# Kernel optimization log

Measured on AMD Instinct MI355X. Metric: run time of the kernel, lower is better.

The kernel has to match this reference:

```python
import jax, jax.numpy as jnp
import numpy as np

DIM = 32
ED = DIM * DIM          # 1024
HID = ED * 4            # 4096
EPS = 1e-5


def _ln(x, g, b):
    # LayerNorm over last two dims (d, d)
    m = x.mean(axis=(-2, -1), keepdims=True)
    v = jnp.var(x, axis=(-2, -1), keepdims=True)
    return (x - m) * jax.lax.rsqrt(v + EPS) * g + b


def setup_inputs() -> dict:
    key = jax.random.key(0)
    ks = jax.random.split(key, 10)
    b, s, d = 2, 1024, DIM
    inp = {
        "x": jax.random.normal(ks[0], (b, s, d, d), dtype=jnp.float32),
        # StateSpaceLayer params
        "log_A": jax.random.normal(ks[1], (d,), dtype=jnp.float32) * 0.02,
        "w_dt": jax.random.normal(ks[2], (d,), dtype=jnp.float32) / np.sqrt(d),
        "b_dt": jnp.zeros((), dtype=jnp.float32),
        "g_ssm": jnp.ones((d, d), dtype=jnp.float32),
        "b_ssm": jnp.zeros((d, d), dtype=jnp.float32),
        # FFN params
        "g_ffn": jnp.ones((d, d), dtype=jnp.float32),
        "b_ffn": jnp.zeros((d, d), dtype=jnp.float32),
        "W1": jax.random.normal(ks[3], (ED, HID), dtype=jnp.float32) / np.sqrt(ED),
        "bb1": jnp.zeros((HID,), dtype=jnp.float32),
        "W2": jax.random.normal(ks[4], (HID, ED), dtype=jnp.float32) / np.sqrt(HID),
        "bb2": jnp.zeros((ED,), dtype=jnp.float32),
    }
    return inp


def reference(x, log_A, w_dt, b_dt, g_ssm, b_ssm, g_ffn, b_ffn, W1, bb1, W2, bb2):
    b, s, d, _ = x.shape
    # ---- StateSpaceLayer (parallel / training path) ----
    xn = _ln(x, g_ssm, b_ssm)                          # (b,s,d,d)
    A_cont = -jnp.exp(log_A)                           # (d,)
    # dt_proj: Linear(d,1) over last axis, then squeeze -> (b,s,d)
    dt = jax.nn.softplus(jnp.einsum('bsrc,c->bsr', xn, w_dt) + b_dt)
    log_a = dt * A_cont                                # (b,s,d)
    cs = jnp.cumsum(log_a, axis=1)                     # (b,s,d)
    log_M = cs[:, :, None, :] - cs[:, None, :, :]      # (b,t,j,d)
    tmask = jnp.arange(s)[:, None] >= jnp.arange(s)[None, :]  # (t,j) causal
    M = jnp.where(tmask[None, :, :, None], jnp.exp(log_M), 0.0)
    ssm_out = jnp.einsum('btjr,bjrc->btrc', M, xn) + x  # residual
    # ---- MatrixFeedForward ----
    fn = _ln(ssm_out, g_ffn, b_ffn).reshape(b, s, d * d)
    h = jax.nn.gelu(fn @ W1 + bb1, approximate=False)
    y = (h @ W2 + bb2).reshape(b, s, d, d)
    return ssm_out + y
```

## Files before the change

### kernel.cpp

```cpp
#include <hip/hip_runtime.h>
#include <math.h>

#define EPSF 1e-5f

typedef __attribute__((ext_vector_type(4))) float f32x4;
typedef __attribute__((ext_vector_type(4))) int i32x4;
typedef __attribute__((ext_vector_type(8))) int i32x8;

__device__ __forceinline__ unsigned short f2bf(float f) {
  unsigned int u = __float_as_uint(f);
  u += 0x7FFFu + ((u >> 16) & 1u);
  return (unsigned short)(u >> 16);
}
__device__ __forceinline__ float bf2f(unsigned short u) {
  return __uint_as_float((unsigned int)u << 16);
}

__device__ __forceinline__ void async_load16(const void* g, void* l) {
  __builtin_amdgcn_global_load_lds(
      (const __attribute__((address_space(1))) void*)g,
      (__attribute__((address_space(3))) void*)l, 16, 0, 0);
}


__device__ __forceinline__ void pack_tile(
    const float* __restrict__ Wsrc, unsigned char* __restrict__ Wdst,
    int WC, int NKW, int bid, int tid, float* smem) {
  int ncg = WC >> 6;
  int c0 = (bid % ncg) * 64, r0 = (bid / ncg) * 64;
  #pragma unroll
  for (int q = 0; q < 4; ++q) {
    int lin = q * 256 + tid;
    int r = lin >> 4, cq = lin & 15;
    float4 v = *(const float4*)(Wsrc + (size_t)(r0 + r) * WC + c0 + cq * 4);
    smem[r * 65 + cq * 4 + 0] = v.x; smem[r * 65 + cq * 4 + 1] = v.y;
    smem[r * 65 + cq * 4 + 2] = v.z; smem[r * 65 + cq * 4 + 3] = v.w;
  }
  __syncthreads();
  int c = tid & 63, kg = tid >> 6;
  int n = c0 + c;
  int k0 = r0 + kg * 16;
  int pk[4];
  #pragma unroll
  for (int q = 0; q < 4; ++q) {
    int p = __builtin_amdgcn_cvt_pk_fp8_f32(
        smem[(kg * 16 + q * 4 + 0) * 65 + c] * 16.0f,
        smem[(kg * 16 + q * 4 + 1) * 65 + c] * 16.0f, 0, false);
    pk[q] = __builtin_amdgcn_cvt_pk_fp8_f32(
        smem[(kg * 16 + q * 4 + 2) * 65 + c] * 16.0f,
        smem[(kg * 16 + q * 4 + 3) * 65 + c] * 16.0f, p, true);
  }
  size_t sb = (size_t)(n >> 4) * NKW + (k0 >> 7);
  int l = ((k0 >> 5) & 3) * 16 + (n & 15);
  int4 o4; o4.x = pk[0]; o4.y = pk[1]; o4.z = pk[2]; o4.w = pk[3];
  *(int4*)(Wdst + sb * 2048 + ((k0 >> 4) & 1) * 1024 + l * 16) = o4;
}

__global__ __launch_bounds__(256) void k_ln1(
    const float* __restrict__ x, const float* __restrict__ g, const float* __restrict__ bta,
    const float* __restrict__ w_dt, const float* __restrict__ b_dt,
    const float* __restrict__ log_A, unsigned short* __restrict__ xn,
    float* __restrict__ log_a) {
  __shared__ float red[8];
  int bs = blockIdx.x;
  int t = threadIdx.x;
  float4 v = ((const float4*)(x + (size_t)bs * 1024))[t];
  float s = v.x + v.y + v.z + v.w;
  float ss = v.x * v.x + v.y * v.y + v.z * v.z + v.w * v.w;
  #pragma unroll
  for (int o = 1; o < 64; o <<= 1) { s += __shfl_xor(s, o); ss += __shfl_xor(ss, o); }
  int w = t >> 6;
  if ((t & 63) == 0) { red[w] = s; red[4 + w] = ss; }
  __syncthreads();
  float S = red[0] + red[1] + red[2] + red[3];
  float SS = red[4] + red[5] + red[6] + red[7];
  float m = S * (1.0f / 1024.0f);
  float var = SS * (1.0f / 1024.0f) - m * m;
  float inv = rsqrtf(var + EPSF);
  float4 gv = ((const float4*)g)[t];
  float4 bv = ((const float4*)bta)[t];
  float4 o;
  o.x = (v.x - m) * inv * gv.x + bv.x;
  o.y = (v.y - m) * inv * gv.y + bv.y;
  o.z = (v.z - m) * inv * gv.z + bv.z;
  o.w = (v.w - m) * inv * gv.w + bv.w;
  ushort4 ob;
  ob.x = f2bf(o.x); ob.y = f2bf(o.y); ob.z = f2bf(o.z); ob.w = f2bf(o.w);
  ((ushort4*)(xn + (size_t)bs * 1024))[t] = ob;
  float4 wv = ((const float4*)w_dt)[t & 7];
  float part = o.x * wv.x + o.y * wv.y + o.z * wv.z + o.w * wv.w;
  part += __shfl_xor(part, 1);
  part += __shfl_xor(part, 2);
  part += __shfl_xor(part, 4);
  if ((t & 7) == 0) {
    int r = t >> 3;
    float z = part + b_dt[0];
    float sp = (z > 20.0f) ? z : log1pf(expf(z));
    log_a[(size_t)bs * 32 + r] = sp * (-expf(log_A[r]));
  }
}

template <int PASS, int NKW>
__global__ __launch_bounds__(256) void k_scan_pack(
    const unsigned short* __restrict__ xn, const float* __restrict__ x,
    const float* __restrict__ loga, float4* __restrict__ E, float* __restrict__ P,
    const float* __restrict__ bb2, float* __restrict__ out,
    const float* __restrict__ Wsrc, unsigned char* __restrict__ Wdst, int WC) {
  __shared__ __align__(16) float smem[64 * 65];
  int tid = threadIdx.x;
  if (blockIdx.x >= 512) {
    pack_tile(Wsrc, Wdst, WC, NKW, blockIdx.x - 512, tid, smem);
    return;
  }
  float* dec = smem;
  float4* sE = (float4*)(smem + 128);
  float* sP = smem + 128 + 1024;
  int bx = blockIdx.x;
  int b = bx >> 8, r = (bx >> 3) & 31, ch = bx & 7;
  int cg = tid & 7, sub = tid >> 3;
  if (tid < 128)
    dec[tid] = expf(loga[(size_t)(b * 1024 + ch * 128 + tid) * 32 + r]);
  __syncthreads();
  int t0 = ch * 128 + sub * 4;
  size_t base = ((size_t)(b * 1024 + t0) * 1024 + r * 32 + cg * 4) >> 2;
  const ushort4* xn4 = (const ushort4*)xn;
  float4 xv[4];
  #pragma unroll
  for (int i = 0; i < 4; ++i) {
    ushort4 u = xn4[base + (size_t)i * 256];
    xv[i].x = bf2f(u.x); xv[i].y = bf2f(u.y); xv[i].z = bf2f(u.z); xv[i].w = bf2f(u.w);
  }
  float4 S = {0.f, 0.f, 0.f, 0.f};
  float Pl = 1.0f;
  #pragma unroll
  for (int i = 0; i < 4; ++i) {
    float d = dec[sub * 4 + i];
    S.x = d * S.x + xv[i].x; S.y = d * S.y + xv[i].y;
    S.z = d * S.z + xv[i].z; S.w = d * S.w + xv[i].w;
    Pl *= d;
  }
  sE[sub * 8 + cg] = S;
  if (cg == 0) sP[sub] = Pl;
  __syncthreads();
  if (PASS == 0) {
    if (tid < 8) {
      float4 Et = {0.f, 0.f, 0.f, 0.f};
      float PP = 1.0f;
      #pragma unroll
      for (int h = 0; h < 32; ++h) {
        float p = sP[h]; float4 e = sE[h * 8 + tid];
        Et.x = p * Et.x + e.x; Et.y = p * Et.y + e.y;
        Et.z = p * Et.z + e.z; Et.w = p * Et.w + e.w;
        PP *= p;
      }
      E[((size_t)(b * 32 + r) * 8 + ch) * 8 + tid] = Et;
      if (tid == 0) P[(b * 32 + r) * 8 + ch] = PP;
    }
  } else {
    float4 Sin = {0.f, 0.f, 0.f, 0.f};
    const float4* Eb = E + (size_t)(b * 32 + r) * 64 + cg;
    const float* Pb = P + (size_t)(b * 32 + r) * 8;
    for (int h = 0; h < ch; ++h) {
      float p = Pb[h]; float4 e = Eb[h * 8];
      Sin.x = p * Sin.x + e.x; Sin.y = p * Sin.y + e.y;
      Sin.z = p * Sin.z + e.z; Sin.w = p * Sin.w + e.w;
    }
    for (int h = 0; h < sub; ++h) {
      float p = sP[h]; float4 e = sE[h * 8 + cg];
      Sin.x = p * Sin.x + e.x; Sin.y = p * Sin.y + e.y;
      Sin.z = p * Sin.z + e.z; Sin.w = p * Sin.w + e.w;
    }
    float4 bb = ((const float4*)bb2)[r * 8 + cg];
    const float4* x4 = (const float4*)x;
    float4* out4 = (float4*)out;
    #pragma unroll
    for (int i = 0; i < 4; ++i) {
      float d = dec[sub * 4 + i];
      Sin.x = d * Sin.x + xv[i].x; Sin.y = d * Sin.y + xv[i].y;
      Sin.z = d * Sin.z + xv[i].z; Sin.w = d * Sin.w + xv[i].w;
      float4 rx = x4[base + (size_t)i * 256];
      float4 oi;
      oi.x = Sin.x + rx.x + bb.x; oi.y = Sin.y + rx.y + bb.y;
      oi.z = Sin.z + rx.z + bb.z; oi.w = Sin.w + rx.w + bb.w;
      out4[base + (size_t)i * 256] = oi;
    }
  }
}

__global__ __launch_bounds__(256) void k_ln2_pack(
    const float* __restrict__ out, const float* __restrict__ bb2,
    const float* __restrict__ g, const float* __restrict__ bta,
    unsigned char* __restrict__ fn,
    const float* __restrict__ W1, unsigned char* __restrict__ W1t) {
  __shared__ __align__(16) unsigned char sC[16640];
  int tid = threadIdx.x;
  if (blockIdx.x >= 128) {
    pack_tile(W1, W1t, 4096, 8, blockIdx.x - 128, tid, (float*)sC);
    return;
  }
  int t15 = tid >> 4;
  int kc = tid & 15;
  int tok = (blockIdx.x << 4) + t15;
  const float4* row = (const float4*)(out + (size_t)tok * 1024);
  const float4* b4 = (const float4*)bb2;
  float4 v[16];
  float s = 0.f, ss = 0.f;
  #pragma unroll
  for (int ci = 0; ci < 4; ++ci) {
    int cc = kc + ci * 16;
    #pragma unroll
    for (int q = 0; q < 4; ++q) {
      float4 xv = row[cc * 4 + q];
      float4 bb = b4[cc * 4 + q];
      xv.x -= bb.x; xv.y -= bb.y; xv.z -= bb.z; xv.w -= bb.w;
      v[ci * 4 + q] = xv;
      s += xv.x + xv.y + xv.z + xv.w;
      ss += xv.x * xv.x + xv.y * xv.y + xv.z * xv.z + xv.w * xv.w;
    }
  }
  #pragma unroll
  for (int o = 1; o < 16; o <<= 1) { s += __shfl_xor(s, o); ss += __shfl_xor(ss, o); }
  float m = s * (1.0f / 1024.0f);
  float var = ss * (1.0f / 1024.0f) - m * m;
  float inv = rsqrtf(var + EPSF);
  #pragma unroll
  for (int ci = 0; ci < 4; ++ci) {
    int cc = kc + ci * 16;
    int pk[4];
    #pragma unroll
    for (int q = 0; q < 4; ++q) {
      float4 gv = ((const float4*)g)[cc * 4 + q];
      float4 bv = ((const float4*)bta)[cc * 4 + q];
      float4 xv = v[ci * 4 + q];
      float f0 = (xv.x - m) * inv * gv.x + bv.x;
      float f1 = (xv.y - m) * inv * gv.y + bv.y;
      float f2 = (xv.z - m) * inv * gv.z + bv.z;
      float f3 = (xv.w - m) * inv * gv.w + bv.w;
      int p = __builtin_amdgcn_cvt_pk_fp8_f32(f0, f1, 0, false);
      pk[q] = __builtin_amdgcn_cvt_pk_fp8_f32(f2, f3, p, true);
    }
    int loc = (cc >> 3) * 2048 + (cc & 1) * 1024 + (((cc >> 1) & 3) * 16 + t15) * 16;
    loc ^= ((loc >> 8) & 7) << 4;
    int4 o4; o4.x = pk[0]; o4.y = pk[1]; o4.z = pk[2]; o4.w = pk[3];
    *(int4*)(sC + loc) = o4;
  }
  __syncthreads();
  unsigned char* dst = fn + (size_t)blockIdx.x * 16384;
  #pragma unroll
  for (int p = 0; p < 4; ++p) {
    int a = (p * 256 + tid) * 16;
    int sa = a ^ (((a >> 8) & 7) << 4);
    *(int4*)(dst + a) = *(const int4*)(sC + sa);
  }
}

__global__ __launch_bounds__(256, 2) void k_gemm1(
    const unsigned char* __restrict__ Ap, const unsigned char* __restrict__ Bp,
    const float* __restrict__ bias, unsigned char* __restrict__ C8) {
  __shared__ __align__(16) unsigned char sAB[65536];
  int L = blockIdx.x;
  int xcd = L & 7;
  int nq = xcd & 3, mh = xcd >> 2;
  int rest = L >> 3;
  int nx = rest & 7, my = rest >> 3;
  int n0 = (nq * 8 + nx) * 128;
  int m0 = (mh * 8 + my) * 128;
  int tid = threadIdx.x;
  int wave = tid >> 6, lane = tid & 63;
  int wr = wave >> 1, wc = wave & 1;
  int l15 = lane & 15, quad = lane >> 4;

  f32x4 zero = {0.0f, 0.0f, 0.0f, 0.0f};
  f32x4 acc[4][4];
  #pragma unroll
  for (int i = 0; i < 4; ++i)
    #pragma unroll
    for (int j = 0; j < 4; ++j) acc[i][j] = zero;

  const unsigned char* gsrc = (wave < 2) ? Ap : Bp;
  int rt0 = (wave < 2) ? (m0 >> 4) : (n0 >> 4);
  int aoff = (wave < 2) ? 0 : 16384;
  int w01 = wave & 1;

  #pragma unroll
  for (int t = 0; t < 8; ++t) {
    int idx = w01 * 8 + t, rt = idx >> 1, h = idx & 1;
    async_load16(gsrc + ((size_t)(rt0 + rt) * 8 + 0) * 2048 + h * 1024 + lane * 16,
                 sAB + aoff + rt * 2048 + h * 1024 + lane * 16);
  }

  #pragma unroll 1
  for (int st = 0; st < 8; ++st) {
    int cur = (st & 1) * 32768;
    if (st < 7) {
      int nxt = cur ^ 32768;
      #pragma unroll
      for (int t = 0; t < 8; ++t) {
        int idx = w01 * 8 + t, rt = idx >> 1, h = idx & 1;
        async_load16(gsrc + ((size_t)(rt0 + rt) * 8 + st + 1) * 2048 + h * 1024 + lane * 16,
                     sAB + nxt + aoff + rt * 2048 + h * 1024 + lane * 16);
      }
      asm volatile("s_waitcnt vmcnt(8)" ::: "memory");
    } else {
      asm volatile("s_waitcnt vmcnt(0)" ::: "memory");
    }
    __builtin_amdgcn_s_barrier();
    const unsigned char* sA = sAB + cur;
    const unsigned char* sB = sAB + cur + 16384;
    i32x8 af[4], bf[4];
    #pragma unroll
    for (int i = 0; i < 4; ++i) {
      const unsigned char* pa = sA + (wr * 4 + i) * 2048 + lane * 16;
      i32x4 lo = *(const i32x4*)pa;
      i32x4 hi = *(const i32x4*)(pa + 1024);
      af[i] = __builtin_shufflevector(lo, hi, 0, 1, 2, 3, 4, 5, 6, 7);
    }
    #pragma unroll
    for (int j = 0; j < 4; ++j) {
      const unsigned char* pb = sB + (wc * 4 + j) * 2048 + lane * 16;
      i32x4 lo = *(const i32x4*)pb;
      i32x4 hi = *(const i32x4*)(pb + 1024);
      bf[j] = __builtin_shufflevector(lo, hi, 0, 1, 2, 3, 4, 5, 6, 7);
    }
    #pragma unroll
    for (int i = 0; i < 4; ++i)
      #pragma unroll
      for (int j = 0; j < 4; ++j)
        acc[i][j] = __builtin_amdgcn_mfma_scale_f32_16x16x128_f8f6f4(
            af[i], bf[j], acc[i][j], 0, 0, 0, 0x7F7F7F7F, 0, 0x7F7F7F7F);
    asm volatile("s_waitcnt lgkmcnt(0)" ::: "memory");
    __builtin_amdgcn_s_barrier();
  }

  unsigned char* sC = sAB;
  #pragma unroll
  for (int i = 0; i < 4; ++i) {
    #pragma unroll
    for (int j = 0; j < 4; ++j) {
      int col_l = wc * 64 + j * 16 + l15;
      float bval = bias[n0 + col_l];
      int half2 = (col_l >> 4) & 1, lb = (col_l >> 5) & 3;
      unsigned char* ld = sC + (wr * 4 + i) * 2048 + half2 * 1024 +
                          (lb * 16 + quad * 4) * 16 + l15;
      float vv[4];
      #pragma unroll
      for (int v = 0; v < 4; ++v) {
        float val = acc[i][j][v] * 0.0625f + bval;
        float u = val * (0.7978845608f + 0.035677408f * val * val);
        vv[v] = val / (1.0f + __expf(-2.0f * u));
      }
      int p01 = __builtin_amdgcn_cvt_pk_fp8_f32(vv[0], vv[1], 0, false);
      int p23 = __builtin_amdgcn_cvt_pk_fp8_f32(vv[2], vv[3], 0, false);
      ld[0 * 16] = (unsigned char)(p01 & 0xff);
      ld[1 * 16] = (unsigned char)((p01 >> 8) & 0xff);
      ld[2 * 16] = (unsigned char)(p23 & 0xff);
      ld[3 * 16] = (unsigned char)((p23 >> 8) & 0xff);
    }
  }
  __syncthreads();
  int mt2_0 = m0 >> 4, kp2 = n0 >> 7;
  #pragma unroll
  for (int p = 0; p < 4; ++p) {
    int ci = p * 256 + tid;
    int s = ci >> 7, off = (ci & 127) * 16;
    *(int4*)(C8 + ((size_t)(mt2_0 + s) * 32 + kp2) * 2048 + off) =
        *(const int4*)(sC + s * 2048 + off);
  }
}

__global__ __launch_bounds__(256, 2) void k_gemm2(
    const unsigned char* __restrict__ Ap, const unsigned char* __restrict__ Bp,
    float* __restrict__ O) {
  __shared__ __align__(16) unsigned char sAB[65536];
  int L = blockIdx.x;
  int xcd = L & 7;
  int mq = xcd >> 1, nh = xcd & 1;
  int rest = L >> 3;
  int nx = rest & 7, my = rest >> 3;
  int n0 = (nh * 8 + nx) * 64;
  int m0 = (mq * 8 + my) * 64;
  int tid = threadIdx.x;
  int wave = tid >> 6, lane = tid & 63;
  int wr = wave >> 1, wc = wave & 1;
  int l15 = lane & 15, quad = lane >> 4;

  f32x4 zero = {0.0f, 0.0f, 0.0f, 0.0f};
  f32x4 acc[2][2];
  #pragma unroll
  for (int i = 0; i < 2; ++i)
    #pragma unroll
    for (int j = 0; j < 2; ++j) acc[i][j] = zero;

  const unsigned char* gsrc = (wave < 2) ? Ap : Bp;
  int rt0 = (wave < 2) ? (m0 >> 4) : (n0 >> 4);
  int aoff = (wave < 2) ? 0 : 16384;
  int w01 = wave & 1;

  #pragma unroll
  for (int t = 0; t < 8; ++t) {
    int idx = w01 * 8 + t, sb = idx >> 1, h = idx & 1;
    int rt = sb >> 1, kt = sb & 1;
    async_load16(gsrc + ((size_t)(rt0 + rt) * 32 + kt) * 2048 + h * 1024 + lane * 16,
                 sAB + aoff + sb * 2048 + h * 1024 + lane * 16);
  }

  #pragma unroll 1
  for (int st = 0; st < 16; ++st) {
    int cur = (st & 1) * 32768;
    if (st < 15) {
      int nxt = cur ^ 32768;
      #pragma unroll
      for (int t = 0; t < 8; ++t) {
        int idx = w01 * 8 + t, sb = idx >> 1, h = idx & 1;
        int rt = sb >> 1, kt = sb & 1;
        async_load16(
            gsrc + ((size_t)(rt0 + rt) * 32 + (st + 1) * 2 + kt) * 2048 + h * 1024 + lane * 16,
            sAB + nxt + aoff + sb * 2048 + h * 1024 + lane * 16);
      }
      asm volatile("s_waitcnt vmcnt(8)" ::: "memory");
    } else {
      asm volatile("s_waitcnt vmcnt(0)" ::: "memory");
    }
    __builtin_amdgcn_s_barrier();
    const unsigned char* sA = sAB + cur;
    const unsigned char* sB = sAB + cur + 16384;
    #pragma unroll
    for (int kl = 0; kl < 2; ++kl) {
      i32x8 af[2], bf[2];
      #pragma unroll
      for (int i = 0; i < 2; ++i) {
        const unsigned char* pa = sA + ((wr * 2 + i) * 2 + kl) * 2048 + lane * 16;
        i32x4 lo = *(const i32x4*)pa;
        i32x4 hi = *(const i32x4*)(pa + 1024);
        af[i] = __builtin_shufflevector(lo, hi, 0, 1, 2, 3, 4, 5, 6, 7);
      }
      #pragma unroll
      for (int j = 0; j < 2; ++j) {
        const unsigned char* pb = sB + ((wc * 2 + j) * 2 + kl) * 2048 + lane * 16;
        i32x4 lo = *(const i32x4*)pb;
        i32x4 hi = *(const i32x4*)(pb + 1024);
        bf[j] = __builtin_shufflevector(lo, hi, 0, 1, 2, 3, 4, 5, 6, 7);
      }
      #pragma unroll
      for (int i = 0; i < 2; ++i)
        #pragma unroll
        for (int j = 0; j < 2; ++j)
          acc[i][j] = __builtin_amdgcn_mfma_scale_f32_16x16x128_f8f6f4(
              af[i], bf[j], acc[i][j], 0, 0, 0, 0x7F7F7F7F, 0, 0x7F7F7F7F);
    }
    asm volatile("s_waitcnt lgkmcnt(0)" ::: "memory");
    __builtin_amdgcn_s_barrier();
  }

  #pragma unroll
  for (int i = 0; i < 2; ++i)
    #pragma unroll
    for (int j = 0; j < 2; ++j) {
      int col = n0 + wc * 32 + j * 16 + l15;
      #pragma unroll
      for (int v = 0; v < 4; ++v) {
        int row = m0 + wr * 32 + i * 16 + quad * 4 + v;
        float* p = &O[(size_t)row * 1024 + col];
        *p = *p + acc[i][j][v] * 0.0625f;
      }
    }
}

extern "C" void kernel_launch(void* const* d_in, const int* in_sizes, int n_in,
                              void* d_out, int out_size, void* d_ws, size_t ws_size,
                              hipStream_t stream) {
  const float* x     = (const float*)d_in[0];
  const float* log_A = (const float*)d_in[1];
  const float* w_dt  = (const float*)d_in[2];
  const float* b_dt  = (const float*)d_in[3];
  const float* g_ssm = (const float*)d_in[4];
  const float* b_ssm = (const float*)d_in[5];
  const float* g_ffn = (const float*)d_in[6];
  const float* b_ffn = (const float*)d_in[7];
  const float* W1    = (const float*)d_in[8];
  const float* bb1   = (const float*)d_in[9];
  const float* W2    = (const float*)d_in[10];
  const float* bb2   = (const float*)d_in[11];
  float* out = (float*)d_out;

  const size_t MB = 1u << 20;
  char* ws = (char*)d_ws;
  unsigned short* xn   = (unsigned short*)(ws);
  unsigned char* W1t   = (unsigned char*)(ws + 4 * MB);
  float* loga          = (float*)(ws + 8 * MB);
  float4* Ebuf         = (float4*)(ws + 8 * MB + 262144);
  float* Pbuf          = (float*)(ws + 8 * MB + 393216);
  unsigned char* fn    = (unsigned char*)(ws + 9 * MB);
  unsigned char* W2t   = (unsigned char*)(ws + 11 * MB);
  unsigned char* hbf   = (unsigned char*)(ws + 15 * MB);

  k_ln1<<<2048, 256, 0, stream>>>(x, g_ssm, b_ssm, w_dt, b_dt, log_A, xn, loga);
  k_scan_pack<0, 8><<<512, 256, 0, stream>>>(xn, x, loga, Ebuf, Pbuf, bb2, out,
                                             W1, W1t, 4096);
  k_scan_pack<1, 32><<<1536, 256, 0, stream>>>(xn, x, loga, Ebuf, Pbuf, bb2, out,
                                               W2, W2t, 1024);
  k_ln2_pack<<<1152, 256, 0, stream>>>(out, bb2, g_ffn, b_ffn, fn, W1, W1t);
  k_gemm1<<<512, 256, 0, stream>>>(fn, W1t, bb1, hbf);
  k_gemm2<<<512, 256, 0, stream>>>(hbf, W2t, out);
}
```

Before: 150.7 us.

## Fuse LN1, scan passes and LN2 into one persistent kernel with grid barriers

Merges four front-end launches (LN1, both scan passes, LN2 pack) into a single kernel. The first 512 blocks sync through software grid barriers on atomic counters, and the scan hand-off uses per-chunk decoupled-lookback flags instead of a separate second pass. The remaining blocks pack W1/W2 to fp8 alongside. This removes launch gaps and the redundant recompute of the scan in pass 1. In exchange it relies on all 512 barrier blocks being co-resident, since packing blocks with higher indices could otherwise starve them, and it adds a memset plus spin-wait overhead.

New measurement: 278.6 us. 84.9% more time.

```diff
diff --git a/kernel.cpp b/kernel.cpp
--- a/kernel.cpp
+++ b/kernel.cpp
@@ -56,78 +56,107 @@
   *(int4*)(Wdst + sb * 2048 + ((k0 >> 4) & 1) * 1024 + l * 16) = o4;
 }
 
-__global__ __launch_bounds__(256) void k_ln1(
-    const float* __restrict__ x, const float* __restrict__ g, const float* __restrict__ bta,
+__device__ __forceinline__ void gbar(int* cnt) {
+  __syncthreads();
+  if (threadIdx.x == 0) {
+    __threadfence();
+    atomicAdd(cnt, 1);
+    while (atomicAdd(cnt, 0) < 512) {}
+    __threadfence();
+  }
+  __syncthreads();
+}
+
+__global__ __launch_bounds__(256) void k_front(
+    const float* __restrict__ x, const float* __restrict__ g1, const float* __restrict__ b1,
     const float* __restrict__ w_dt, const float* __restrict__ b_dt,
     const float* __restrict__ log_A, unsigned short* __restrict__ xn,
-    float* __restrict__ log_a) {
-  __shared__ float red[8];
-  int bs = blockIdx.x;
-  int t = threadIdx.x;
-  float4 v = ((const float4*)(x + (size_t)bs * 1024))[t];
-  float s = v.x + v.y + v.z + v.w;
-  float ss = v.x * v.x + v.y * v.y + v.z * v.z + v.w * v.w;
-  #pragma unroll
-  for (int o = 1; o < 64; o <<= 1) { s += __shfl_xor(s, o); ss += __shfl_xor(ss, o); }
-  int w = t >> 6;
-  if ((t & 63) == 0) { red[w] = s; red[4 + w] = ss; }
-  __syncthreads();
-  float S = red[0] + red[1] + red[2] + red[3];
-  float SS = red[4] + red[5] + red[6] + red[7];
-  float m = S * (1.0f / 1024.0f);
-  float var = SS * (1.0f / 1024.0f) - m * m;
-  float inv = rsqrtf(var + EPSF);
-  float4 gv = ((const float4*)g)[t];
-  float4 bv = ((const float4*)bta)[t];
-  float4 o;
-  o.x = (v.x - m) * inv * gv.x + bv.x;
-  o.y = (v.y - m) * inv * gv.y + bv.y;
-  o.z = (v.z - m) * inv * gv.z + bv.z;
-  o.w = (v.w - m) * inv * gv.w + bv.w;
-  ushort4 ob;
-  ob.x = f2bf(o.x); ob.y = f2bf(o.y); ob.z = f2bf(o.z); ob.w = f2bf(o.w);
-  ((ushort4*)(xn + (size_t)bs * 1024))[t] = ob;
-  float4 wv = ((const float4*)w_dt)[t & 7];
-  float part = o.x * wv.x + o.y * wv.y + o.z * wv.z + o.w * wv.w;
-  part += __shfl_xor(part, 1);
-  part += __shfl_xor(part, 2);
-  part += __shfl_xor(part, 4);
-  if ((t & 7) == 0) {
-    int r = t >> 3;
-    float z = part + b_dt[0];
-    float sp = (z > 20.0f) ? z : log1pf(expf(z));
-    log_a[(size_t)bs * 32 + r] = sp * (-expf(log_A[r]));
-  }
-}
-
-template <int PASS, int NKW>
-__global__ __launch_bounds__(256) void k_scan_pack(
-    const unsigned short* __restrict__ xn, const float* __restrict__ x,
-    const float* __restrict__ loga, float4* __restrict__ E, float* __restrict__ P,
+    float* __restrict__ log_a, float4* __restrict__ E, float* __restrict__ P,
     const float* __restrict__ bb2, float* __restrict__ out,
-    const float* __restrict__ Wsrc, unsigned char* __restrict__ Wdst, int WC) {
+    const float* __restrict__ g2, const float* __restrict__ b2,
+    unsigned char* __restrict__ fn,
+    const float* __restrict__ W1, unsigned char* __restrict__ W1t,
+    const float* __restrict__ W2, unsigned char* __restrict__ W2t,
+    int* __restrict__ flags) {
   __shared__ __align__(16) float smem[64 * 65];
   int tid = threadIdx.x;
-  if (blockIdx.x >= 512) {
-    pack_tile(Wsrc, Wdst, WC, NKW, blockIdx.x - 512, tid, smem);
+  int bx = blockIdx.x;
+  if (bx >= 512) {
+    int bid = bx - 512;
+    if (bid < 1024) pack_tile(W1, W1t, 4096, 8, bid, tid, smem);
+    else            pack_tile(W2, W2t, 1024, 32, bid - 1024, tid, smem);
     return;
   }
+
+  {
+    int sub = tid >> 6, l = tid & 63;
+    int tok = bx * 4 + sub;
+    const float4* xr = (const float4*)(x + (size_t)tok * 1024);
+    float4 v[4];
+    float s = 0.f, ss = 0.f;
+    #pragma unroll
+    for (int q = 0; q < 4; ++q) {
+      v[q] = xr[l + 64 * q];
+      s += v[q].x + v[q].y + v[q].z + v[q].w;
+      ss += v[q].x * v[q].x + v[q].y * v[q].y + v[q].z * v[q].z + v[q].w * v[q].w;
+    }
+    #pragma unroll
+    for (int o = 1; o < 64; o <<= 1) { s += __shfl_xor(s, o); ss += __shfl_xor(ss, o); }
+    float m = s * (1.0f / 1024.0f);
+    float var = ss * (1.0f / 1024.0f) - m * m;
+    float inv = rsqrtf(var + EPSF);
+    float4 wv = ((const float4*)w_dt)[l & 7];
+    float part[4];
+    ushort4* xn4 = (ushort4*)xn;
+    #pragma unroll
+    for (int q = 0; q < 4; ++q) {
+      float4 gv = ((const float4*)g1)[l + 64 * q];
+      float4 bv = ((const float4*)b1)[l + 64 * q];
+      float4 o;
+      o.x = (v[q].x - m) * inv * gv.x + bv.x;
+      o.y = (v[q].y - m) * inv * gv.y + bv.y;
+      o.z = (v[q].z - m) * inv * gv.z + bv.z;
+      o.w = (v[q].w - m) * inv * gv.w + bv.w;
+      ushort4 ob;
+      ob.x = f2bf(o.x); ob.y = f2bf(o.y); ob.z = f2bf(o.z); ob.w = f2bf(o.w);
+      xn4[(size_t)tok * 256 + l + 64 * q] = ob;
+      part[q] = o.x * wv.x + o.y * wv.y + o.z * wv.z + o.w * wv.w;
+    }
+    #pragma unroll
+    for (int o = 1; o < 8; o <<= 1) {
+      #pragma unroll
+      for (int q = 0; q < 4; ++q) part[q] += __shfl_xor(part[q], o);
+    }
+    if ((l & 7) == 0) {
+      int mrow = l >> 3;
+      #pragma unroll
+      for (int q = 0; q < 4; ++q) {
+        int r = mrow + 8 * q;
+        float z = part[q] + b_dt[0];
+        float sp = (z > 20.0f) ? z : log1pf(expf(z));
+        log_a[(size_t)tok * 32 + r] = sp * (-expf(log_A[r]));
+      }
+    }
+  }
+
+  gbar(flags + 0);
+
   float* dec = smem;
   float4* sE = (float4*)(smem + 128);
   float* sP = smem + 128 + 1024;
-  int bx = blockIdx.x;
+  int* lkf = flags + 16;
   int b = bx >> 8, r = (bx >> 3) & 31, ch = bx & 7;
   int cg = tid & 7, sub = tid >> 3;
   if (tid < 128)
-    dec[tid] = expf(loga[(size_t)(b * 1024 + ch * 128 + tid) * 32 + r]);
+    dec[tid] = expf(log_a[(size_t)(b * 1024 + ch * 128 + tid) * 32 + r]);
   __syncthreads();
   int t0 = ch * 128 + sub * 4;
   size_t base = ((size_t)(b * 1024 + t0) * 1024 + r * 32 + cg * 4) >> 2;
-  const ushort4* xn4 = (const ushort4*)xn;
+  const ushort4* xn4c = (const ushort4*)xn;
   float4 xv[4];
   #pragma unroll
   for (int i = 0; i < 4; ++i) {
-    ushort4 u = xn4[base + (size_t)i * 256];
+    ushort4 u = xn4c[base + (size_t)i * 256];
     xv[i].x = bf2f(u.x); xv[i].y = bf2f(u.y); xv[i].z = bf2f(u.z); xv[i].w = bf2f(u.w);
   }
   float4 S = {0.f, 0.f, 0.f, 0.f};
@@ -142,21 +171,30 @@
   sE[sub * 8 + cg] = S;
   if (cg == 0) sP[sub] = Pl;
   __syncthreads();
-  if (PASS == 0) {
-    if (tid < 8) {
-      float4 Et = {0.f, 0.f, 0.f, 0.f};
-      float PP = 1.0f;
-      #pragma unroll
-      for (int h = 0; h < 32; ++h) {
-        float p = sP[h]; float4 e = sE[h * 8 + tid];
-        Et.x = p * Et.x + e.x; Et.y = p * Et.y + e.y;
-        Et.z = p * Et.z + e.z; Et.w = p * Et.w + e.w;
-        PP *= p;
-      }
-      E[((size_t)(b * 32 + r) * 8 + ch) * 8 + tid] = Et;
-      if (tid == 0) P[(b * 32 + r) * 8 + ch] = PP;
-    }
-  } else {
+  if (tid < 8) {
+    float4 Et = {0.f, 0.f, 0.f, 0.f};
+    float PP = 1.0f;
+    #pragma unroll
+    for (int h = 0; h < 32; ++h) {
+      float p = sP[h]; float4 e = sE[h * 8 + tid];
+      Et.x = p * Et.x + e.x; Et.y = p * Et.y + e.y;
+      Et.z = p * Et.z + e.z; Et.w = p * Et.w + e.w;
+      PP *= p;
+    }
+    E[((size_t)(b * 32 + r) * 8 + ch) * 8 + tid] = Et;
+    if (tid == 0) P[(b * 32 + r) * 8 + ch] = PP;
+  }
+  __syncthreads();
+  int lkbase = (b * 32 + r) * 8;
+  if (tid == 0) {
+    __threadfence();
+    atomicExch(&lkf[lkbase + ch], 1);
+    for (int h = 0; h < ch; ++h)
+      while (atomicAdd(&lkf[lkbase + h], 0) == 0) {}
+    __threadfence();
+  }
+  __syncthreads();
+  {
     float4 Sin = {0.f, 0.f, 0.f, 0.f};
     const float4* Eb = E + (size_t)(b * 32 + r) * 64 + cg;
     const float* Pb = P + (size_t)(b * 32 + r) * 8;
@@ -185,72 +223,65 @@
       out4[base + (size_t)i * 256] = oi;
     }
   }
-}
-
-__global__ __launch_bounds__(256) void k_ln2_pack(
-    const float* __restrict__ out, const float* __restrict__ bb2,
-    const float* __restrict__ g, const float* __restrict__ bta,
-    unsigned char* __restrict__ fn,
-    const float* __restrict__ W1, unsigned char* __restrict__ W1t) {
-  __shared__ __align__(16) unsigned char sC[16640];
-  int tid = threadIdx.x;
-  if (blockIdx.x >= 128) {
-    pack_tile(W1, W1t, 4096, 8, blockIdx.x - 128, tid, (float*)sC);
-    return;
-  }
-  int t15 = tid >> 4;
-  int kc = tid & 15;
-  int tok = (blockIdx.x << 4) + t15;
-  const float4* row = (const float4*)(out + (size_t)tok * 1024);
-  const float4* b4 = (const float4*)bb2;
-  float4 v[16];
-  float s = 0.f, ss = 0.f;
-  #pragma unroll
-  for (int ci = 0; ci < 4; ++ci) {
-    int cc = kc + ci * 16;
-    #pragma unroll
-    for (int q = 0; q < 4; ++q) {
-      float4 xv = row[cc * 4 + q];
-      float4 bb = b4[cc * 4 + q];
-      xv.x -= bb.x; xv.y -= bb.y; xv.z -= bb.z; xv.w -= bb.w;
-      v[ci * 4 + q] = xv;
-      s += xv.x + xv.y + xv.z + xv.w;
-      ss += xv.x * xv.x + xv.y * xv.y + xv.z * xv.z + xv.w * xv.w;
-    }
-  }
-  #pragma unroll
-  for (int o = 1; o < 16; o <<= 1) { s += __shfl_xor(s, o); ss += __shfl_xor(ss, o); }
-  float m = s * (1.0f / 1024.0f);
-  float var = ss * (1.0f / 1024.0f) - m * m;
-  float inv = rsqrtf(var + EPSF);
-  #pragma unroll
-  for (int ci = 0; ci < 4; ++ci) {
-    int cc = kc + ci * 16;
-    int pk[4];
-    #pragma unroll
-    for (int q = 0; q < 4; ++q) {
-      float4 gv = ((const float4*)g)[cc * 4 + q];
-      float4 bv = ((const float4*)bta)[cc * 4 + q];
-      float4 xv = v[ci * 4 + q];
-      float f0 = (xv.x - m) * inv * gv.x + bv.x;
-      float f1 = (xv.y - m) * inv * gv.y + bv.y;
-      float f2 = (xv.z - m) * inv * gv.z + bv.z;
-      float f3 = (xv.w - m) * inv * gv.w + bv.w;
-      int p = __builtin_amdgcn_cvt_pk_fp8_f32(f0, f1, 0, false);
-      pk[q] = __builtin_amdgcn_cvt_pk_fp8_f32(f2, f3, p, true);
-    }
-    int loc = (cc >> 3) * 2048 + (cc & 1) * 1024 + (((cc >> 1) & 3) * 16 + t15) * 16;
-    loc ^= ((loc >> 8) & 7) << 4;
-    int4 o4; o4.x = pk[0]; o4.y = pk[1]; o4.z = pk[2]; o4.w = pk[3];
-    *(int4*)(sC + loc) = o4;
-  }
-  __syncthreads();
-  unsigned char* dst = fn + (size_t)blockIdx.x * 16384;
-  #pragma unroll
-  for (int p = 0; p < 4; ++p) {
-    int a = (p * 256 + tid) * 16;
-    int sa = a ^ (((a >> 8) & 7) << 4);
-    *(int4*)(dst + a) = *(const int4*)(sC + sa);
+
+  gbar(flags + 1);
+
+  if (bx < 128) {
+    unsigned char* sC = (unsigned char*)smem;
+    int t15 = tid >> 4;
+    int kc = tid & 15;
+    int tok = (bx << 4) + t15;
+    const float4* row = (const float4*)(out + (size_t)tok * 1024);
+    const float4* b4 = (const float4*)bb2;
+    float4 v[16];
+    float s = 0.f, ss = 0.f;
+    #pragma unroll
+    for (int ci = 0; ci < 4; ++ci) {
+      int cc = kc + ci * 16;
+      #pragma unroll
+      for (int q = 0; q < 4; ++q) {
+        float4 xv2 = row[cc * 4 + q];
+        float4 bb = b4[cc * 4 + q];
+        xv2.x -= bb.x; xv2.y -= bb.y; xv2.z -= bb.z; xv2.w -= bb.w;
+        v[ci * 4 + q] = xv2;
+        s += xv2.x + xv2.y + xv2.z + xv2.w;
+        ss += xv2.x * xv2.x + xv2.y * xv2.y + xv2.z * xv2.z + xv2.w * xv2.w;
+      }
+    }
+    #pragma unroll
+    for (int o = 1; o < 16; o <<= 1) { s += __shfl_xor(s, o); ss += __shfl_xor(ss, o); }
+    float m = s * (1.0f / 1024.0f);
+    float var = ss * (1.0f / 1024.0f) - m * m;
+    float inv = rsqrtf(var + EPSF);
+    #pragma unroll
+    for (int ci = 0; ci < 4; ++ci) {
+      int cc = kc + ci * 16;
+      int pk[4];
+      #pragma unroll
+      for (int q = 0; q < 4; ++q) {
+        float4 gv = ((const float4*)g2)[cc * 4 + q];
+        float4 bv = ((const float4*)b2)[cc * 4 + q];
+        float4 xv2 = v[ci * 4 + q];
+        float f0 = (xv2.x - m) * inv * gv.x + bv.x;
+        float f1 = (xv2.y - m) * inv * gv.y + bv.y;
+        float f2 = (xv2.z - m) * inv * gv.z + bv.z;
+        float f3 = (xv2.w - m) * inv * gv.w + bv.w;
+        int p = __builtin_amdgcn_cvt_pk_fp8_f32(f0, f1, 0, false);
+        pk[q] = __builtin_amdgcn_cvt_pk_fp8_f32(f2, f3, p, true);
+      }
+      int loc = (cc >> 3) * 2048 + (cc & 1) * 1024 + (((cc >> 1) & 3) * 16 + t15) * 16;
+      loc ^= ((loc >> 8) & 7) << 4;
+      int4 o4; o4.x = pk[0]; o4.y = pk[1]; o4.z = pk[2]; o4.w = pk[3];
+      *(int4*)(sC + loc) = o4;
+    }
+    __syncthreads();
+    unsigned char* dst = fn + (size_t)bx * 16384;
+    #pragma unroll
+    for (int p = 0; p < 4; ++p) {
+      int a = (p * 256 + tid) * 16;
+      int sa = a ^ (((a >> 8) & 7) << 4);
+      *(int4*)(dst + a) = *(const int4*)(sC + sa);
+    }
   }
 }
 
@@ -490,16 +521,15 @@
   float* loga          = (float*)(ws + 8 * MB);
   float4* Ebuf         = (float4*)(ws + 8 * MB + 262144);
   float* Pbuf          = (float*)(ws + 8 * MB + 393216);
+  int* flags           = (int*)(ws + 8 * MB + 409600);
   unsigned char* fn    = (unsigned char*)(ws + 9 * MB);
   unsigned char* W2t   = (unsigned char*)(ws + 11 * MB);
   unsigned char* hbf   = (unsigned char*)(ws + 15 * MB);
 
-  k_ln1<<<2048, 256, 0, stream>>>(x, g_ssm, b_ssm, w_dt, b_dt, log_A, xn, loga);
-  k_scan_pack<0, 8><<<512, 256, 0, stream>>>(xn, x, loga, Ebuf, Pbuf, bb2, out,
-                                             W1, W1t, 4096);
-  k_scan_pack<1, 32><<<1536, 256, 0, stream>>>(xn, x, loga, Ebuf, Pbuf, bb2, out,
-                                               W2, W2t, 1024);
-  k_ln2_pack<<<1152, 256, 0, stream>>>(out, bb2, g_ffn, b_ffn, fn, W1, W1t);
+  hipMemsetAsync(flags, 0, 4096, stream);
+  k_front<<<2560, 256, 0, stream>>>(x, g_ssm, b_ssm, w_dt, b_dt, log_A, xn, loga,
+                                    Ebuf, Pbuf, bb2, out, g_ffn, b_ffn, fn,
+                                    W1, W1t, W2, W2t, flags);
   k_gemm1<<<512, 256, 0, stream>>>(fn, W1t, bb1, hbf);
   k_gemm2<<<512, 256, 0, stream>>>(hbf, W2t, out);
 }
```
